# Kernel optimization log

Measured on AMD Instinct MI355X. Metric: run time of the kernel, lower is better.

## Reference

```python
import jax, jax.numpy as jnp
import numpy as np

NEG_SLOPE = 0.01  # torch F.leaky_relu default


def _leaky_relu(v):
    return jnp.where(v >= 0, v, NEG_SLOPE * v)


def _att_layer(t, w1, w2):
    # t: [b, c, n] ; SE-style channel attention with scalar gate
    y = t.mean(axis=-1)                                   # [b, c] (AdaptiveAvgPool1d(1))
    y = jax.nn.sigmoid(jax.nn.relu(y @ w1.T) @ w2.T)       # [b, 1]
    return t * y[:, :, None]


def _avwgcn(x, node_emb, supports, cheb, wpool, bpool, iw, ib, gw, gb,
            a1w1, a1w2, a2w1, a2w2):
    # x: [b, n, c_in]; supports/cheb: [k, n, n]
    b, n, _ = x.shape
    weights = jnp.einsum('nd,dkio->nkio', node_emb, wpool)   # per-node dyn weights
    bias = node_emb @ bpool                                  # [n, o]
    x_g = jnp.einsum('knm,bmc->bnkc', supports, x)           # [b, n, k, c_in]
    x_gconv0 = jnp.einsum('bnki,nkio->bno', x_g, weights) + bias
    x0 = x @ iw.T + ib                                       # init_gconv: [b, n, o]
    x_g1 = jnp.einsum('knm,bmc->bnkc', cheb, x0).reshape(b, n, -1)
    x_gconv1 = x_g1 @ gw.T + gb                              # [b, n, o]
    out = (_att_layer(_leaky_relu(x_gconv0).transpose(0, 2, 1), a1w1, a1w2)
           + _att_layer(_leaky_relu(x_gconv1).transpose(0, 2, 1), a2w1, a2w2))
    return out.transpose(0, 2, 1)                            # [b, n, o]


def _cheb_supports(L, k):
    n = L.shape[0]
    s = [jnp.eye(n, dtype=L.dtype), L]
    for _ in range(2, k):
        s.append(2.0 * L @ s[-1] - s[-2])
    return jnp.stack(s, axis=0)  # [k, n, n]


B, N, DIN, DOUT, K, ED = 64, 1024, 32, 64, 3, 16
CIN = DIN + DOUT  # 96 (gate/update input = cat(x, state))


def setup_inputs() -> dict:
    key = jax.random.key(0)
    ks = jax.random.split(key, 32)
    g = lambda i, shape, s=0.1: jax.random.normal(ks[i], shape, dtype=jnp.float32) * s
    inp = {
        'x': jax.random.normal(ks[0], (B, N, DIN), dtype=jnp.float32),
        'state': jax.random.normal(ks[1], (B, N, DOUT), dtype=jnp.float32),
        'node_embeddings': jax.random.normal(ks[2], (N, ED), dtype=jnp.float32),
        'learned_tilde': jax.random.normal(ks[3], (N, N), dtype=jnp.float32) / np.sqrt(N),
        'cheb_polynomials': jax.random.normal(ks[4], (K, N, N), dtype=jnp.float32) / np.sqrt(N),
        # gate AVWGCN: dim_in=96, dim_out=2*DOUT=128
        'gate_wpool': g(5, (ED, K, CIN, 2 * DOUT)),
        'gate_bpool': g(6, (ED, 2 * DOUT)),
        'gate_iw': g(7, (2 * DOUT, CIN)), 'gate_ib': g(8, (2 * DOUT,)),
        'gate_gw': g(9, (2 * DOUT, 2 * DOUT * K)), 'gate_gb': g(10, (2 * DOUT,)),
        'gate_a1w1': g(11, (2 * DOUT // 16, 2 * DOUT)), 'gate_a1w2': g(12, (1, 2 * DOUT // 16)),
        'gate_a2w1': g(13, (2 * DOUT // 16, 2 * DOUT)), 'gate_a2w2': g(14, (1, 2 * DOUT // 16)),
        # update AVWGCN: dim_in=96, dim_out=DOUT=64
        'upd_wpool': g(15, (ED, K, CIN, DOUT)),
        'upd_bpool': g(16, (ED, DOUT)),
        'upd_iw': g(17, (DOUT, CIN)), 'upd_ib': g(18, (DOUT,)),
        'upd_gw': g(19, (DOUT, DOUT * K)), 'upd_gb': g(20, (DOUT,)),
        'upd_a1w1': g(21, (DOUT // 16, DOUT)), 'upd_a1w2': g(22, (1, DOUT // 16)),
        'upd_a2w1': g(23, (DOUT // 16, DOUT)), 'upd_a2w2': g(24, (1, DOUT // 16)),
    }
    return inp


def reference(x, state, node_embeddings, learned_tilde, cheb_polynomials,
              gate_wpool, gate_bpool, gate_iw, gate_ib, gate_gw, gate_gb,
              gate_a1w1, gate_a1w2, gate_a2w1, gate_a2w2,
              upd_wpool, upd_bpool, upd_iw, upd_ib, upd_gw, upd_gb,
              upd_a1w1, upd_a1w2, upd_a2w1, upd_a2w2):
    supports = _cheb_supports(learned_tilde, K)  # [k, n, n]
    inp_state = jnp.concatenate([x, state], axis=-1)  # [b, n, din+dout]
    z_r = jax.nn.sigmoid(_avwgcn(inp_state, node_embeddings, supports, cheb_polynomials,
                                 gate_wpool, gate_bpool, gate_iw, gate_ib, gate_gw, gate_gb,
                                 gate_a1w1, gate_a1w2, gate_a2w1, gate_a2w2))
    z, r = jnp.split(z_r, 2, axis=-1)
    candidate = jnp.concatenate([x, z * state], axis=-1)
    hc = jnp.tanh(_avwgcn(candidate, node_embeddings, supports, cheb_polynomials,
                          upd_wpool, upd_bpool, upd_iw, upd_ib, upd_gw, upd_gb,
                          upd_a1w1, upd_a1w2, upd_a2w1, upd_a2w2))
    h = r * state + (1.0 - r) * hc
    return h
```

## Files before the change

kernel.cpp:

```cpp
#include <hip/hip_runtime.h>
#include <hip/hip_bf16.h>
#include <math.h>


#define B_  64
#define N_  1024
#define CIN_ 96
#define R_  288

typedef __attribute__((ext_vector_type(8))) short bf16x8;
typedef __attribute__((ext_vector_type(4))) float f32x4;
typedef unsigned short u16;
typedef unsigned int u32;

__device__ __forceinline__ float lrelu(float v) { return v >= 0.f ? v : 0.01f * v; }
__device__ __forceinline__ float sigmoidf_(float u) { return 1.f / (1.f + expf(-u)); }
__device__ __forceinline__ u16 f2b(float f) {
  union { float f; u32 u; } c; c.f = f;
  u32 u = c.u;
  return (u16)((u + 0x7FFFu + ((u >> 16) & 1u)) >> 16);
}
__device__ __forceinline__ float b2f(u16 u) {
  union { u32 x; float f; } c; c.x = ((u32)u) << 16; return c.f;
}
__device__ __forceinline__ void gload_lds16(const u16* gp, u16* lp) {
  __builtin_amdgcn_global_load_lds((const __attribute__((address_space(1))) u32*)gp,
                                   (__attribute__((address_space(3))) u32*)lp, 16, 0, 0);
}

__global__ __launch_bounds__(256) void concat_bf2(const float* __restrict__ x,
                                                  const float* __restrict__ st,
                                                  float* __restrict__ inp,
                                                  u16* __restrict__ inpb) {
  size_t t = (size_t)blockIdx.x * 256 + threadIdx.x;
  if (t >= (size_t)B_ * N_ * CIN_) return;
  int i = (int)(t % CIN_);
  size_t v = t / CIN_;
  size_t b = v & 63, n = v >> 6;
  float f = (i < 32) ? x[(b * N_ + n) * 32 + i] : st[(b * N_ + n) * 64 + (i - 32)];
  inp[t] = f;
  inpb[t] = f2b(f);
}

__global__ __launch_bounds__(256) void conv_f2b(const float* __restrict__ in,
                                                u16* __restrict__ out, int n4) {
  int t = blockIdx.x * 256 + threadIdx.x;
  if (t >= n4) return;
  float4 v = ((const float4*)in)[t];
  ushort4 o;
  o.x = f2b(v.x); o.y = f2b(v.y); o.z = f2b(v.z); o.w = f2b(v.w);
  ((ushort4*)out)[t] = o;
}

__global__ __launch_bounds__(256) void split_hilo(const float* __restrict__ in,
                                                  u16* __restrict__ hi,
                                                  u16* __restrict__ lo, int n4) {
  int t = blockIdx.x * 256 + threadIdx.x;
  if (t >= n4) return;
  float4 v = ((const float4*)in)[t];
  ushort4 h, l;
  h.x = f2b(v.x); l.x = f2b(v.x - b2f(h.x));
  h.y = f2b(v.y); l.y = f2b(v.y - b2f(h.y));
  h.z = f2b(v.z); l.z = f2b(v.z - b2f(h.z));
  h.w = f2b(v.w); l.w = f2b(v.w - b2f(h.w));
  ((ushort4*)hi)[t] = h;
  ((ushort4*)lo)[t] = l;
}

__global__ __launch_bounds__(256) void transpose_split(const float* __restrict__ in,
                                                       u16* __restrict__ hiT,
                                                       u16* __restrict__ loT) {
  __shared__ float t[32][33];
  const int tid = threadIdx.x;
  const int j0 = blockIdx.x * 32, r0 = blockIdx.y * 32;
  const int tc = tid & 31, tr = tid >> 5;
#pragma unroll
  for (int q = 0; q < 4; ++q)
    t[tr + q * 8][tc] = in[(size_t)(r0 + tr + q * 8) * 1024 + j0 + tc];
  __syncthreads();
  const int jj = tid >> 3, rq = (tid & 7) * 4;
  ushort4 h, l;
#pragma unroll
  for (int q = 0; q < 4; ++q) {
    float v = t[rq + q][jj];
    u16 hh = f2b(v);
    ((u16*)&h)[q] = hh;
    ((u16*)&l)[q] = f2b(v - b2f(hh));
  }
  *(ushort4*)(hiT + (size_t)(j0 + jj) * N_ + r0 + rq) = h;
  *(ushort4*)(loT + (size_t)(j0 + jj) * N_ + r0 + rq) = l;
}

__global__ __launch_bounds__(256) void transpose_b2b(const u16* __restrict__ Z, int Zs,
                                                     int Ctot, u16* __restrict__ Zt) {
  __shared__ u16 t[32][36];
  const int tid = threadIdx.x;
  const int c0 = blockIdx.x * 32, n0 = blockIdx.y * 32, b = blockIdx.z;
  {
    const int i = tid >> 3, c4 = (tid & 7) * 4;
    ushort4 v = *(const ushort4*)(Z + ((size_t)(n0 + i) * 64 + b) * Zs + c0 + c4);
    t[i][c4] = v.x; t[i][c4 + 1] = v.y; t[i][c4 + 2] = v.z; t[i][c4 + 3] = v.w;
  }
  __syncthreads();
  {
    const int c = tid >> 3, n4 = (tid & 7) * 4;
    ushort4 o;
    o.x = t[n4][c]; o.y = t[n4 + 1][c]; o.z = t[n4 + 2][c]; o.w = t[n4 + 3][c];
    *(ushort4*)(Zt + (size_t)(b * Ctot + c0 + c) * 1024 + n0 + n4) = o;
  }
}

__global__ __launch_bounds__(256) void wpool_tr(const float* __restrict__ wp,
                                                float* __restrict__ wpT, int OW) {
  __shared__ float t[32][33];
  const int tid = threadIdx.x;
  const int r0 = blockIdx.x * 32, o0 = blockIdx.y * 32, d = blockIdx.z;
  const size_t base = (size_t)d * 288 * OW;
  const int c = tid & 31, q0 = tid >> 5;
#pragma unroll
  for (int q = 0; q < 4; ++q)
    t[q0 + q * 8][c] = wp[base + (size_t)(r0 + q0 + q * 8) * OW + o0 + c];
  __syncthreads();
#pragma unroll
  for (int q = 0; q < 4; ++q)
    wpT[base + (size_t)(o0 + q0 + q * 8) * 288 + r0 + c] = t[c][q0 + q * 8];
}

__global__ __launch_bounds__(256) void mfma_l2p(const u16* __restrict__ Lhi,
                                                const u16* __restrict__ Llo,
                                                const u16* __restrict__ LhiT,
                                                const u16* __restrict__ LloT,
                                                float* __restrict__ P) {
  __shared__ u16 Asl[64 * 64];
  __shared__ u16 Bsl[64 * 64];
  const int tid = threadIdx.x;
  const int w = tid >> 6, lane = tid & 63;
  const int m0 = blockIdx.y * 64, n0 = blockIdx.x * 64;
  const int ph = blockIdx.z;
  const int wr = w >> 1, wc = w & 1;
  const int sr = lane >> 3, so = lane & 7;
  const int cl = lane & 15, q4 = lane >> 4;
  f32x4 acc[2][2] = {};

  const u16* A = (ph == 1) ? Llo : Lhi;
  const u16* B = (ph == 2) ? LloT : LhiT;
  for (int k0 = 0; k0 < 1024; k0 += 64) {
    __syncthreads();
#pragma unroll
    for (int i = 0; i < 2; ++i) {
      const int r = i * 32 + w * 8 + sr;
      const int o = so ^ (r & 7);
      gload_lds16(A + (size_t)(m0 + r) * 1024 + k0 + o * 8, Asl + (i * 32 + w * 8) * 64);
      gload_lds16(B + (size_t)(n0 + r) * 1024 + k0 + o * 8, Bsl + (i * 32 + w * 8) * 64);
    }
    __syncthreads();
#pragma unroll
    for (int kk = 0; kk < 2; ++kk) {
      bf16x8 af[2], bfr[2];
#pragma unroll
      for (int mi = 0; mi < 2; ++mi) {
        const int ra = wr * 32 + mi * 16 + cl;
        af[mi] = *(const bf16x8*)(Asl + ra * 64 + ((kk * 4 + q4) ^ (ra & 7)) * 8);
      }
#pragma unroll
      for (int ni = 0; ni < 2; ++ni) {
        const int rb = wc * 32 + ni * 16 + cl;
        bfr[ni] = *(const bf16x8*)(Bsl + rb * 64 + ((kk * 4 + q4) ^ (rb & 7)) * 8);
      }
#pragma unroll
      for (int mi = 0; mi < 2; ++mi)
#pragma unroll
        for (int ni = 0; ni < 2; ++ni)
          acc[mi][ni] = __builtin_amdgcn_mfma_f32_16x16x32_bf16(af[mi], bfr[ni], acc[mi][ni], 0, 0, 0);
    }
  }
  float* Pz = P + ((size_t)ph << 20);
#pragma unroll
  for (int mi = 0; mi < 2; ++mi)
#pragma unroll
    for (int ni = 0; ni < 2; ++ni) {
      const int j = n0 + wc * 32 + ni * 16 + cl;
#pragma unroll
      for (int r = 0; r < 4; ++r) {
        const int m = m0 + wr * 32 + mi * 16 + q4 * 4 + r;
        Pz[(size_t)m * 1024 + j] = acc[mi][ni][r];
      }
    }
}

__global__ __launch_bounds__(256) void l2_finish(const float* __restrict__ P,
                                                 u16* __restrict__ Y) {
  int t = blockIdx.x * 256 + threadIdx.x;
  float4 a = ((const float4*)P)[t];
  float4 b = ((const float4*)(P + 1048576))[t];
  float4 c = ((const float4*)(P + 2097152))[t];
  int e = t << 2;
  int m = e >> 10, j = e & 1023;
  ushort4 o;
  o.x = f2b(2.f * (a.x + b.x + c.x) - (m == j     ? 1.f : 0.f));
  o.y = f2b(2.f * (a.y + b.y + c.y) - (m == j + 1 ? 1.f : 0.f));
  o.z = f2b(2.f * (a.z + b.z + c.z) - (m == j + 2 ? 1.f : 0.f));
  o.w = f2b(2.f * (a.w + b.w + c.w) - (m == j + 3 ? 1.f : 0.f));
  ((ushort4*)Y)[t] = o;
}

__global__ __launch_bounds__(512) void mfma_stack_w(const u16* __restrict__ A,
                                                    const u16* __restrict__ Bt,
                                                    float* __restrict__ Y, int J) {
  __shared__ u16 Asl[2][128 * 64];
  __shared__ u16 Bsl[2][256 * 64];
  const int tid = threadIdx.x;
  const int w = tid >> 6, lane = tid & 63;
  const int m0 = blockIdx.y * 128, n0 = blockIdx.x * 256;
  const int wr = w >> 2, wc = w & 3;
  const int sr = lane >> 3, so = lane & 7;
  const int cl = lane & 15, q4 = lane >> 4;
  f32x4 acc[4][4] = {};

  auto STAGE = [&](u16* Ad, u16* Bd, int k0) {
#pragma unroll
    for (int i = 0; i < 2; ++i) {
      const int r = i * 64 + w * 8 + sr;
      const int o = so ^ (r & 7);
      gload_lds16(A + (size_t)(m0 + r) * 1024 + k0 + o * 8, Ad + (i * 64 + w * 8) * 64);
    }
#pragma unroll
    for (int i = 0; i < 4; ++i) {
      const int r = i * 64 + w * 8 + sr;
      const int o = so ^ (r & 7);
      gload_lds16(Bt + (size_t)(n0 + r) * 1024 + k0 + o * 8, Bd + (i * 64 + w * 8) * 64);
    }
  };
  auto COMPUTE = [&](const u16* As, const u16* Bs) {
#pragma unroll
    for (int kk = 0; kk < 2; ++kk) {
      bf16x8 af[4], bfr[4];
#pragma unroll
      for (int mi = 0; mi < 4; ++mi) {
        const int ra = wr * 64 + mi * 16 + cl;
        af[mi] = *(const bf16x8*)(As + ra * 64 + ((kk * 4 + q4) ^ (ra & 7)) * 8);
      }
#pragma unroll
      for (int ni = 0; ni < 4; ++ni) {
        const int rb = wc * 64 + ni * 16 + cl;
        bfr[ni] = *(const bf16x8*)(Bs + rb * 64 + ((kk * 4 + q4) ^ (rb & 7)) * 8);
      }
#pragma unroll
      for (int mi = 0; mi < 4; ++mi)
#pragma unroll
        for (int ni = 0; ni < 4; ++ni)
          acc[mi][ni] = __builtin_amdgcn_mfma_f32_16x16x32_bf16(af[mi], bfr[ni], acc[mi][ni], 0, 0, 0);
    }
  };

  STAGE(Asl[0], Bsl[0], 0);
  for (int k0 = 0; k0 < 1024; k0 += 128) {
    STAGE(Asl[1], Bsl[1], k0 + 64);
    asm volatile("s_waitcnt vmcnt(6)" ::: "memory");
    __builtin_amdgcn_s_barrier();
    __builtin_amdgcn_sched_barrier(0);
    COMPUTE(Asl[0], Bsl[0]);
    asm volatile("s_waitcnt lgkmcnt(0)" ::: "memory");
    __builtin_amdgcn_s_barrier();
    __builtin_amdgcn_sched_barrier(0);
    if (k0 + 128 < 1024) {
      STAGE(Asl[0], Bsl[0], k0 + 128);
      asm volatile("s_waitcnt vmcnt(6)" ::: "memory");
    } else {
      asm volatile("s_waitcnt vmcnt(0)" ::: "memory");
    }
    __builtin_amdgcn_s_barrier();
    __builtin_amdgcn_sched_barrier(0);
    COMPUTE(Asl[1], Bsl[1]);
    asm volatile("s_waitcnt lgkmcnt(0)" ::: "memory");
    __builtin_amdgcn_s_barrier();
    __builtin_amdgcn_sched_barrier(0);
  }
#pragma unroll
  for (int mi = 0; mi < 4; ++mi)
#pragma unroll
    for (int ni = 0; ni < 4; ++ni) {
      const int j = n0 + wc * 64 + ni * 16 + cl;
#pragma unroll
      for (int r = 0; r < 4; ++r) {
        const int m = m0 + wr * 64 + mi * 16 + q4 * 4 + r;
        Y[(size_t)m * J + j] = acc[mi][ni][r];
      }
    }
}

template <int O, int OSH>
__global__ __launch_bounds__(128) void vgen2(const float* __restrict__ gw,
                                             const float* __restrict__ iw,
                                             const float* __restrict__ ib,
                                             int Ctot,
                                             u16* __restrict__ Vb,
                                             float* __restrict__ ball) {
  const int c = blockIdx.x;
  const int col = threadIdx.x;
  if (c >= Ctot) {
    if (col < 96) Vb[(size_t)c * 96 + col] = 0;
    else if (col == 96) ball[c] = 0.f;
    return;
  }
  __shared__ float sg[O];
  const int o = c & (O - 1), k = c >> OSH;
  const float* g = gw + (size_t)o * (3 * O) + (size_t)k * O;
  for (int e = col; e < O; e += 128) sg[e] = g[e];
  __syncthreads();
  if (col < 96) {
    float s = 0.f;
#pragma unroll
    for (int j = 0; j < O; ++j) s += sg[j] * iw[j * 96 + col];
    Vb[(size_t)c * 96 + col] = f2b(s);
  } else if (col == 96) {
    float s = 0.f;
#pragma unroll
    for (int j = 0; j < O; ++j) s += sg[j] * ib[j];
    ball[c] = s;
  }
}

__global__ __launch_bounds__(256) void zgemm(const u16* __restrict__ A,
                                             const u16* __restrict__ Bt,
                                             const float* __restrict__ ball,
                                             u16* __restrict__ Z, int Zs) {
  __shared__ u16 Asl[128 * 32];
  __shared__ u16 Bsl[128 * 32];
  const int tid = threadIdx.x;
  const int w = tid >> 6, lane = tid & 63;
  const int m0 = blockIdx.y * 128, n0 = blockIdx.x * 128;
  const int wr = w >> 1, wc = w & 1;
  const int sr = lane >> 2, so = lane & 3;
  const int cl = lane & 15, q4 = lane >> 4;
  f32x4 acc[4][4] = {};
  for (int k0 = 0; k0 < 96; k0 += 32) {
    __syncthreads();
#pragma unroll
    for (int i = 0; i < 2; ++i) {
      const int r = i * 64 + w * 16 + sr;
      const int o = so ^ (r & 3);
      gload_lds16(A + (size_t)(m0 + r) * 96 + k0 + o * 8, Asl + (i * 64 + w * 16) * 32);
      gload_lds16(Bt + (size_t)(n0 + r) * 96 + k0 + o * 8, Bsl + (i * 64 + w * 16) * 32);
    }
    __syncthreads();
    bf16x8 af[4], bfr[4];
#pragma unroll
    for (int mi = 0; mi < 4; ++mi) {
      const int ra = wr * 64 + mi * 16 + cl;
      af[mi] = *(const bf16x8*)(Asl + ra * 32 + (q4 ^ (ra & 3)) * 8);
    }
#pragma unroll
    for (int ni = 0; ni < 4; ++ni) {
      const int rb = wc * 64 + ni * 16 + cl;
      bfr[ni] = *(const bf16x8*)(Bsl + rb * 32 + (q4 ^ (rb & 3)) * 8);
    }
#pragma unroll
    for (int mi = 0; mi < 4; ++mi)
#pragma unroll
      for (int ni = 0; ni < 4; ++ni)
        acc[mi][ni] = __builtin_amdgcn_mfma_f32_16x16x32_bf16(af[mi], bfr[ni], acc[mi][ni], 0, 0, 0);
  }
#pragma unroll
  for (int mi = 0; mi < 4; ++mi)
#pragma unroll
    for (int ni = 0; ni < 4; ++ni) {
      const int c = n0 + wc * 64 + ni * 16 + cl;
      const float bb = ball[c];
#pragma unroll
      for (int r = 0; r < 4; ++r) {
        const int m = m0 + wr * 64 + mi * 16 + q4 * 4 + r;
        Z[(size_t)m * Zs + c] = f2b(acc[mi][ni][r] + bb);
      }
    }
}

__global__ __launch_bounds__(512) void mfma_k3(const u16* __restrict__ A3,
                                               const u16* __restrict__ Zt,
                                               const float* __restrict__ gb,
                                               float* __restrict__ Y,
                                               int J, int obits) {
  __shared__ u16 Asl[2][128 * 64];
  __shared__ u16 Bsl[2][128 * 64];
  const int tid = threadIdx.x;
  const int w = tid >> 6, lane = tid & 63;
  const int m0 = blockIdx.y * 128, n0 = blockIdx.x * 128;
  const int wr = w >> 2, wc = w & 3;
  const int sr = lane >> 3, so = lane & 7;
  const int cl = lane & 15, q4 = lane >> 4;
  const int omask = (1 << obits) - 1;
  f32x4 acc[4][2] = {};

  auto STAGE = [&](u16* Ad, u16* Bd, int k0) {
    const int kb = k0 >> 10, ko = k0 & 1023;
#pragma unroll
    for (int i = 0; i < 2; ++i) {
      const int r = i * 64 + w * 8 + sr;
      const int o = so ^ (r & 7);
      gload_lds16(A3 + (size_t)kb * 1048576 + (size_t)(m0 + r) * 1024 + ko + o * 8,
                  Ad + (i * 64 + w * 8) * 64);
      const int jp = n0 + r;
      const int brow = (((jp >> obits) * 3 + kb) << obits) | (jp & omask);
      gload_lds16(Zt + (size_t)brow * 1024 + ko + o * 8, Bd + (i * 64 + w * 8) * 64);
    }
  };
  auto COMPUTE = [&](const u16* As, const u16* Bs) {
#pragma unroll
    for (int kk = 0; kk < 2; ++kk) {
      bf16x8 af[4], bfr[2];
#pragma unroll
      for (int mi = 0; mi < 4; ++mi) {
        const int ra = wr * 64 + mi * 16 + cl;
        af[mi] = *(const bf16x8*)(As + ra * 64 + ((kk * 4 + q4) ^ (ra & 7)) * 8);
      }
#pragma unroll
      for (int ni = 0; ni < 2; ++ni) {
        const int rb = wc * 32 + ni * 16 + cl;
        bfr[ni] = *(const bf16x8*)(Bs + rb * 64 + ((kk * 4 + q4) ^ (rb & 7)) * 8);
      }
#pragma unroll
      for (int mi = 0; mi < 4; ++mi)
#pragma unroll
        for (int ni = 0; ni < 2; ++ni)
          acc[mi][ni] = __builtin_amdgcn_mfma_f32_16x16x32_bf16(af[mi], bfr[ni], acc[mi][ni], 0, 0, 0);
    }
  };

  STAGE(Asl[0], Bsl[0], 0);
  for (int k0 = 0; k0 < 3072; k0 += 128) {
    STAGE(Asl[1], Bsl[1], k0 + 64);
    asm volatile("s_waitcnt vmcnt(4)" ::: "memory");
    __builtin_amdgcn_s_barrier();
    __builtin_amdgcn_sched_barrier(0);
    COMPUTE(Asl[0], Bsl[0]);
    asm volatile("s_waitcnt lgkmcnt(0)" ::: "memory");
    __builtin_amdgcn_s_barrier();
    __builtin_amdgcn_sched_barrier(0);
    if (k0 + 128 < 3072) {
      STAGE(Asl[0], Bsl[0], k0 + 128);
      asm volatile("s_waitcnt vmcnt(4)" ::: "memory");
    } else {
      asm volatile("s_waitcnt vmcnt(0)" ::: "memory");
    }
    __builtin_amdgcn_s_barrier();
    __builtin_amdgcn_sched_barrier(0);
    COMPUTE(Asl[1], Bsl[1]);
    asm volatile("s_waitcnt lgkmcnt(0)" ::: "memory");
    __builtin_amdgcn_s_barrier();
    __builtin_amdgcn_sched_barrier(0);
  }
#pragma unroll
  for (int mi = 0; mi < 4; ++mi)
#pragma unroll
    for (int ni = 0; ni < 2; ++ni) {
      const int j = n0 + wc * 32 + ni * 16 + cl;
      const float bb = gb[j & omask];
#pragma unroll
      for (int r = 0; r < 4; ++r) {
        const int m = m0 + wr * 64 + mi * 16 + q4 * 4 + r;
        Y[(size_t)m * J + j] = acc[mi][ni][r] + bb;
      }
    }
}

__global__ __launch_bounds__(512) void mfma_k3w(const u16* __restrict__ A3,
                                                const u16* __restrict__ Zt,
                                                const float* __restrict__ gb,
                                                float* __restrict__ Y,
                                                int J, int obits) {
  __shared__ u16 Asl[2][128 * 64];
  __shared__ u16 Bsl[2][256 * 64];
  const int tid = threadIdx.x;
  const int w = tid >> 6, lane = tid & 63;
  const int m0 = blockIdx.y * 128, n0 = blockIdx.x * 256;
  const int wr = w >> 2, wc = w & 3;
  const int sr = lane >> 3, so = lane & 7;
  const int cl = lane & 15, q4 = lane >> 4;
  const int omask = (1 << obits) - 1;
  f32x4 acc[4][4] = {};

  auto STAGE = [&](u16* Ad, u16* Bd, int k0) {
    const int kb = k0 >> 10, ko = k0 & 1023;
#pragma unroll
    for (int i = 0; i < 2; ++i) {
      const int r = i * 64 + w * 8 + sr;
      const int o = so ^ (r & 7);
      gload_lds16(A3 + (size_t)kb * 1048576 + (size_t)(m0 + r) * 1024 + ko + o * 8,
                  Ad + (i * 64 + w * 8) * 64);
    }
#pragma unroll
    for (int i = 0; i < 4; ++i) {
      const int r = i * 64 + w * 8 + sr;
      const int o = so ^ (r & 7);
      const int jp = n0 + r;
      const int brow = (((jp >> obits) * 3 + kb) << obits) | (jp & omask);
      gload_lds16(Zt + (size_t)brow * 1024 + ko + o * 8, Bd + (i * 64 + w * 8) * 64);
    }
  };
  auto COMPUTE = [&](const u16* As, const u16* Bs) {
#pragma unroll
    for (int kk = 0; kk < 2; ++kk) {
      bf16x8 af[4], bfr[4];
#pragma unroll
      for (int mi = 0; mi < 4; ++mi) {
        const int ra = wr * 64 + mi * 16 + cl;
        af[mi] = *(const bf16x8*)(As + ra * 64 + ((kk * 4 + q4) ^ (ra & 7)) * 8);
      }
#pragma unroll
      for (int ni = 0; ni < 4; ++ni) {
        const int rb = wc * 64 + ni * 16 + cl;
        bfr[ni] = *(const bf16x8*)(Bs + rb * 64 + ((kk * 4 + q4) ^ (rb & 7)) * 8);
      }
#pragma unroll
      for (int mi = 0; mi < 4; ++mi)
#pragma unroll
        for (int ni = 0; ni < 4; ++ni)
          acc[mi][ni] = __builtin_amdgcn_mfma_f32_16x16x32_bf16(af[mi], bfr[ni], acc[mi][ni], 0, 0, 0);
    }
  };

  STAGE(Asl[0], Bsl[0], 0);
  for (int k0 = 0; k0 < 3072; k0 += 128) {
    STAGE(Asl[1], Bsl[1], k0 + 64);
    asm volatile("s_waitcnt vmcnt(6)" ::: "memory");
    __builtin_amdgcn_s_barrier();
    __builtin_amdgcn_sched_barrier(0);
    COMPUTE(Asl[0], Bsl[0]);
    asm volatile("s_waitcnt lgkmcnt(0)" ::: "memory");
    __builtin_amdgcn_s_barrier();
    __builtin_amdgcn_sched_barrier(0);
    if (k0 + 128 < 3072) {
      STAGE(Asl[0], Bsl[0], k0 + 128);
      asm volatile("s_waitcnt vmcnt(6)" ::: "memory");
    } else {
      asm volatile("s_waitcnt vmcnt(0)" ::: "memory");
    }
    __builtin_amdgcn_s_barrier();
    __builtin_amdgcn_sched_barrier(0);
    COMPUTE(Asl[1], Bsl[1]);
    asm volatile("s_waitcnt lgkmcnt(0)" ::: "memory");
    __builtin_amdgcn_s_barrier();
    __builtin_amdgcn_sched_barrier(0);
  }
#pragma unroll
  for (int mi = 0; mi < 4; ++mi)
#pragma unroll
    for (int ni = 0; ni < 4; ++ni) {
      const int j = n0 + wc * 64 + ni * 16 + cl;
      const float bb = gb[j & omask];
#pragma unroll
      for (int r = 0; r < 4; ++r) {
        const int m = m0 + wr * 64 + mi * 16 + q4 * 4 + r;
        Y[(size_t)m * J + j] = acc[mi][ni][r] + bb;
      }
    }
}

template <int SZ>
__global__ __launch_bounds__(256) void weightgen5(const float* __restrict__ emb,
                                                  const float* __restrict__ wpT,
                                                  u16* __restrict__ W) {
  const int tid = threadIdx.x;
  const int ro = blockIdx.x * 256 + tid;
  const int n0 = blockIdx.y * 64;
  __shared__ float semb[64][17];
  for (int e = tid; e < 1024; e += 256) semb[e >> 4][e & 15] = emb[(n0 + (e >> 4)) * 16 + (e & 15)];
  __syncthreads();
  float wv[16];
#pragma unroll
  for (int d = 0; d < 16; ++d) wv[d] = wpT[(size_t)d * SZ + ro];
#pragma unroll 4
  for (int n = 0; n < 64; ++n) {
    float s = 0.f;
#pragma unroll
    for (int d = 0; d < 16; ++d) s += semb[n][d] * wv[d];
    W[(size_t)(n0 + n) * SZ + ro] = f2b(s);
  }
}

template <int OW>
__global__ __launch_bounds__(256) void pernode10(const float* __restrict__ xa,
                                                 const float* __restrict__ xbc,
                                                 const u16* __restrict__ Wt,
                                                 const float* __restrict__ emb,
                                                 const float* __restrict__ bpool,
                                                 float* __restrict__ outp) {
  constexpr int MT = OW / 64;
  const int n = blockIdx.x;
  const int tid = threadIdx.x;
  const int w = tid >> 6, lane = tid & 63;
  const int cl = lane & 15, q4 = lane >> 4;
  __shared__ u16 sWt[OW * 32];
  __shared__ u16 sXh[64 * 32];
  __shared__ u16 sXl[64 * 32];
  __shared__ float semb[16];
  if (tid < 16) semb[tid] = emb[n * 16 + tid];
  f32x4 acc[MT][4] = {};
  const u16* Wn = Wt + (size_t)n * (OW * 288);
  const int xb = tid >> 2, rg = tid & 3;

  for (int c = 0; c < 9; ++c) {
    const int k = c / 3, i0 = (c % 3) * 32;
    const float* xk = (k == 0) ? (xa + (size_t)n * 6144)
                               : (xbc + ((size_t)(k - 1) * 1024 + n) * 6144);
    __syncthreads();
#pragma unroll
    for (int i = 0; i < MT; ++i) {
      const int g = w * MT + i;
      const int o = g * 16 + (lane >> 2);
      const int seg = (lane & 3) ^ (o & 3);
      gload_lds16(Wn + (size_t)o * 288 + c * 32 + seg * 8, sWt + g * 512);
    }
    {
      const float* p = xk + (size_t)xb * 96 + i0 + rg * 8;
      float4 v0 = *(const float4*)p;
      float4 v1 = *(const float4*)(p + 4);
      float xv[8] = {v0.x, v0.y, v0.z, v0.w, v1.x, v1.y, v1.z, v1.w};
      bf16x8 h, l;
#pragma unroll
      for (int j = 0; j < 8; ++j) {
        u16 hh = f2b(xv[j]);
        ((u16*)&h)[j] = hh;
        ((u16*)&l)[j] = f2b(xv[j] - b2f(hh));
      }
      const int col = (rg ^ (xb & 3)) * 8;
      *(bf16x8*)(sXh + xb * 32 + col) = h;
      *(bf16x8*)(sXl + xb * 32 + col) = l;
    }
    __syncthreads();
    bf16x8 aw[MT], bh[4], bl[4];
#pragma unroll
    for (int mi = 0; mi < MT; ++mi) {
      const int o = (w * MT + mi) * 16 + cl;
      aw[mi] = *(const bf16x8*)(sWt + o * 32 + ((q4 ^ (o & 3)) * 8));
    }
#pragma unroll
    for (int ni = 0; ni < 4; ++ni) {
      const int b = ni * 16 + cl;
      const int col = (q4 ^ (b & 3)) * 8;
      bh[ni] = *(const bf16x8*)(sXh + b * 32 + col);
      bl[ni] = *(const bf16x8*)(sXl + b * 32 + col);
    }
#pragma unroll
    for (int mi = 0; mi < MT; ++mi)
#pragma unroll
      for (int ni = 0; ni < 4; ++ni)
        acc[mi][ni] = __builtin_amdgcn_mfma_f32_16x16x32_bf16(aw[mi], bh[ni], acc[mi][ni], 0, 0, 0);
#pragma unroll
    for (int mi = 0; mi < MT; ++mi)
#pragma unroll
      for (int ni = 0; ni < 4; ++ni)
        acc[mi][ni] = __builtin_amdgcn_mfma_f32_16x16x32_bf16(aw[mi], bl[ni], acc[mi][ni], 0, 0, 0);
  }
  float4 biasv[MT];
#pragma unroll
  for (int mi = 0; mi < MT; ++mi)
#pragma unroll
    for (int r = 0; r < 4; ++r) {
      const int o = (w * MT + mi) * 16 + q4 * 4 + r;
      float s = 0.f;
#pragma unroll
      for (int d = 0; d < 16; ++d) s += semb[d] * bpool[d * OW + o];
      ((float*)&biasv[mi])[r] = s;
    }
#pragma unroll
  for (int mi = 0; mi < MT; ++mi)
#pragma unroll
    for (int ni = 0; ni < 4; ++ni) {
      const int b = ni * 16 + cl;
      float4 v;
      v.x = acc[mi][ni][0] + biasv[mi].x;
      v.y = acc[mi][ni][1] + biasv[mi].y;
      v.z = acc[mi][ni][2] + biasv[mi].z;
      v.w = acc[mi][ni][3] + biasv[mi].w;
      *(float4*)(outp + ((size_t)n * 64 + b) * OW + (w * MT + mi) * 16 + q4 * 4) = v;
    }
}

template <int C>
__global__ __launch_bounds__(256) void att_reduce(const float* __restrict__ A0,
                                                  const float* __restrict__ A1,
                                                  float* __restrict__ part0,
                                                  float* __restrict__ part1) {
  constexpr int C4 = C / 4;
  constexpr int H = 256 / C4;
  const int chunk = blockIdx.x;
  const int b = blockIdx.y;
  const int tid = threadIdx.x;
  const int c4 = tid % C4, h = tid / C4;
  __shared__ float4 r0[256], r1[256];
  float4 s0 = {0.f, 0.f, 0.f, 0.f}, s1 = {0.f, 0.f, 0.f, 0.f};
  const float4* p0 = (const float4*)(A0 + (size_t)b * C) + c4;
  const float4* p1 = (const float4*)(A1 + (size_t)b * C) + c4;
  const size_t stride = (size_t)B_ * C4;
  for (int n = chunk * 64 + h; n < chunk * 64 + 64; n += H) {
    float4 v0 = p0[(size_t)n * stride];
    float4 v1 = p1[(size_t)n * stride];
    s0.x += lrelu(v0.x); s0.y += lrelu(v0.y); s0.z += lrelu(v0.z); s0.w += lrelu(v0.w);
    s1.x += lrelu(v1.x); s1.y += lrelu(v1.y); s1.z += lrelu(v1.z); s1.w += lrelu(v1.w);
  }
  r0[tid] = s0; r1[tid] = s1;
  __syncthreads();
  if (h == 0) {
    for (int hh = 1; hh < H; ++hh) {
      float4 a = r0[c4 + hh * C4], bb = r1[c4 + hh * C4];
      s0.x += a.x; s0.y += a.y; s0.z += a.z; s0.w += a.w;
      s1.x += bb.x; s1.y += bb.y; s1.z += bb.z; s1.w += bb.w;
    }
    ((float4*)(part0 + ((size_t)b * 16 + chunk) * C))[c4] = s0;
    ((float4*)(part1 + ((size_t)b * 16 + chunk) * C))[c4] = s1;
  }
}

template <int C, int HID>
__global__ __launch_bounds__(256) void att_finish(const float* __restrict__ part0,
                                                  const float* __restrict__ part1,
                                                  const float* __restrict__ w11,
                                                  const float* __restrict__ w12,
                                                  const float* __restrict__ w21,
                                                  const float* __restrict__ w22,
                                                  float* __restrict__ sout) {
  const int b = blockIdx.x;
  const int tid = threadIdx.x;
  __shared__ float sm0[C], sm1[C];
  __shared__ float h0[HID], h1[HID];
  if (tid < C) {
    float s0 = 0.f, s1 = 0.f;
    for (int ch = 0; ch < 16; ++ch) {
      s0 += part0[((size_t)b * 16 + ch) * C + tid];
      s1 += part1[((size_t)b * 16 + ch) * C + tid];
    }
    sm0[tid] = s0 * (1.f / N_); sm1[tid] = s1 * (1.f / N_);
  }
  __syncthreads();
  if (tid < HID) {
    float a = 0.f;
    for (int cc = 0; cc < C; ++cc) a += sm0[cc] * w11[tid * C + cc];
    h0[tid] = fmaxf(a, 0.f);
  } else if (tid >= 32 && tid < 32 + HID) {
    int j = tid - 32;
    float a = 0.f;
    for (int cc = 0; cc < C; ++cc) a += sm1[cc] * w21[j * C + cc];
    h1[j] = fmaxf(a, 0.f);
  }
  __syncthreads();
  if (tid == 0) {
    float a = 0.f;
    for (int j = 0; j < HID; ++j) a += h0[j] * w12[j];
    sout[b] = sigmoidf_(a);
  } else if (tid == 32) {
    float a = 0.f;
    for (int j = 0; j < HID; ++j) a += h1[j] * w22[j];
    sout[B_ + b] = sigmoidf_(a);
  }
}

__global__ __launch_bounds__(256) void gate_combine_b2(const float* __restrict__ a0,
                                                       const float* __restrict__ a1,
                                                       const float* __restrict__ s12,
                                                       const float* __restrict__ x,
                                                       const float* __restrict__ st,
                                                       float* __restrict__ cand,
                                                       u16* __restrict__ candb,
                                                       float* __restrict__ rbuf) {
  size_t t = (size_t)blockIdx.x * 256 + threadIdx.x;
  if (t >= (size_t)B_ * N_ * 64) return;
  int c = (int)(t & 63);
  int b = (int)((t >> 6) & 63);
  int n = (int)(t >> 12);
  float s1 = s12[b], s2 = s12[B_ + b];
  size_t nb = (size_t)n * B_ + b;
  size_t i128 = nb * 128;
  float uz = s1 * lrelu(a0[i128 + c]) + s2 * lrelu(a1[i128 + c]);
  float ur = s1 * lrelu(a0[i128 + 64 + c]) + s2 * lrelu(a1[i128 + 64 + c]);
  float z = sigmoidf_(uz);
  float r = sigmoidf_(ur);
  float stv = st[((size_t)b * N_ + n) * 64 + c];
  float zs = z * stv;
  cand[nb * CIN_ + 32 + c] = zs;
  candb[nb * CIN_ + 32 + c] = f2b(zs);
  rbuf[nb * 64 + c] = r;
  if (c < 32) {
    float xv = x[((size_t)b * N_ + n) * 32 + c];
    cand[nb * CIN_ + c] = xv;
    candb[nb * CIN_ + c] = f2b(xv);
  }
}

__global__ __launch_bounds__(256) void final_h(const float* __restrict__ a0,
                                               const float* __restrict__ a1,
                                               const float* __restrict__ s12,
                                               const float* __restrict__ rbuf,
                                               const float* __restrict__ st,
                                               float* __restrict__ out) {
  size_t t = (size_t)blockIdx.x * 256 + threadIdx.x;
  if (t >= (size_t)B_ * N_ * 64) return;
  int o = (int)(t & 63);
  int n = (int)((t >> 6) & 1023);
  int b = (int)(t >> 16);
  float s1 = s12[b], s2 = s12[B_ + b];
  size_t nb = ((size_t)n * B_ + b) * 64 + o;
  float u = s1 * lrelu(a0[nb]) + s2 * lrelu(a1[nb]);
  float hc = tanhf(u);
  float r = rbuf[nb];
  out[t] = r * st[t] + (1.f - r) * hc;
}

extern "C" void kernel_launch(void* const* d_in, const int* in_sizes, int n_in,
                              void* d_out, int out_size, void* d_ws, size_t ws_size,
                              hipStream_t stream) {
  const float* x       = (const float*)d_in[0];
  const float* state   = (const float*)d_in[1];
  const float* emb     = (const float*)d_in[2];
  const float* Ltil    = (const float*)d_in[3];
  const float* cheb    = (const float*)d_in[4];
  const float* g_wpool = (const float*)d_in[5];
  const float* g_bpool = (const float*)d_in[6];
  const float* g_iw    = (const float*)d_in[7];
  const float* g_ib    = (const float*)d_in[8];
  const float* g_gw    = (const float*)d_in[9];
  const float* g_gb    = (const float*)d_in[10];
  const float* g_a1w1  = (const float*)d_in[11];
  const float* g_a1w2  = (const float*)d_in[12];
  const float* g_a2w1  = (const float*)d_in[13];
  const float* g_a2w2  = (const float*)d_in[14];
  const float* u_wpool = (const float*)d_in[15];
  const float* u_bpool = (const float*)d_in[16];
  const float* u_iw    = (const float*)d_in[17];
  const float* u_ib    = (const float*)d_in[18];
  const float* u_gw    = (const float*)d_in[19];
  const float* u_gb    = (const float*)d_in[20];
  const float* u_a1w1  = (const float*)d_in[21];
  const float* u_a1w2  = (const float*)d_in[22];
  const float* u_a2w1  = (const float*)d_in[23];
  const float* u_a2w2  = (const float*)d_in[24];
  float* out = (float*)d_out;

  float* ws    = (float*)d_ws;
  float* inp   = ws;
  u16*   inpb  = (u16*)(ws + 6291456);
  float* t12   = ws + 9437184;
  u16*   Zbuf  = (u16*)t12;
  u16*   Wbuf  = (u16*)(ws + 22020096);
  u16*   Wbuf128 = Wbuf;
  u16*   Btp   = (u16*)(ws + 31457280);
  u16*   Zt    = Wbuf;
  float* acc1  = ws + 34603008;
  float* acc0  = ws + 42991616;
  u16*   LbStk = (u16*)(ws + 51380224);
  u16*   chebb = (u16*)(ws + 52428800);
  float* s12   = ws + 54001664;
  float* s12u  = ws + 54001792;
  float* part0 = ws + 54001920;
  float* part1 = ws + 54132992;
  float* rbuf  = ws + 54264064;
  u16*   Vbg   = (u16*)(ws + 58458368);
  float* bag   = ws + 58476800;
  u16*   Vbu   = (u16*)(ws + 58477184);
  float* bau   = ws + 58489472;
  u16*   LhiT  = (u16*)(ws + 58489728);
  u16*   LloT  = (u16*)(ws + 59014016);
  u16*   Llo   = (u16*)(ws + 59538304);
  float* wpTg  = ws + 58489728;
  float* wpTu  = ws + 59079552;

  dim3 blk(256);
  dim3 blk512(512);

  split_hilo<<<1024, blk, 0, stream>>>(Ltil, LbStk, Llo, 262144);
  transpose_split<<<dim3(32, 32), blk, 0, stream>>>(Ltil, LhiT, LloT);
  mfma_l2p<<<dim3(16, 16, 3), blk, 0, stream>>>(LbStk, Llo, LhiT, LloT, t12);
  wpool_tr<<<dim3(9, 4, 16), blk, 0, stream>>>(g_wpool, wpTg, 128);
  wpool_tr<<<dim3(9, 2, 16), blk, 0, stream>>>(u_wpool, wpTu, 64);
  l2_finish<<<1024, blk, 0, stream>>>(t12, LbStk + 1048576);
  conv_f2b<<<3072, blk, 0, stream>>>(cheb, chebb, 786432);

  concat_bf2<<<24576, blk, 0, stream>>>(x, state, inp, inpb);
  transpose_b2b<<<dim3(3, 32, 64), blk, 0, stream>>>(inpb, 96, 96, Btp);
  mfma_stack_w<<<dim3(24, 16), blk512, 0, stream>>>(LbStk, Btp, t12, 6144);
  vgen2<128, 7><<<384, dim3(128), 0, stream>>>(g_gw, g_iw, g_ib, 384, Vbg, bag);
  weightgen5<36864><<<dim3(144, 16), blk, 0, stream>>>(emb, wpTg, Wbuf128);
  pernode10<128><<<1024, blk, 0, stream>>>(inp, t12, Wbuf128, emb, g_bpool, acc0);
  zgemm<<<dim3(3, 512), blk, 0, stream>>>(inpb, Vbg, bag, Zbuf, 384);
  transpose_b2b<<<dim3(12, 32, 64), blk, 0, stream>>>(Zbuf, 384, 384, Zt);
  mfma_k3w<<<dim3(32, 8), blk512, 0, stream>>>(chebb, Zt, g_gb, acc1, 8192, 7);
  att_reduce<128><<<dim3(16, 64), blk, 0, stream>>>(acc0, acc1, part0, part1);
  att_finish<128, 8><<<64, blk, 0, stream>>>(part0, part1, g_a1w1, g_a1w2, g_a2w1, g_a2w2, s12);
  gate_combine_b2<<<16384, blk, 0, stream>>>(acc0, acc1, s12, x, state, inp, inpb, rbuf);

  transpose_b2b<<<dim3(3, 32, 64), blk, 0, stream>>>(inpb, 96, 96, Btp);
  mfma_stack_w<<<dim3(24, 16), blk512, 0, stream>>>(LbStk, Btp, t12, 6144);
  vgen2<64, 6><<<256, dim3(128), 0, stream>>>(u_gw, u_iw, u_ib, 192, Vbu, bau);
  weightgen5<18432><<<dim3(72, 16), blk, 0, stream>>>(emb, wpTu, Wbuf);
  pernode10<64><<<1024, blk, 0, stream>>>(inp, t12, Wbuf, emb, u_bpool, acc0);
  zgemm<<<dim3(2, 512), blk, 0, stream>>>(inpb, Vbu, bau, Zbuf, 256);
  transpose_b2b<<<dim3(6, 32, 64), blk, 0, stream>>>(Zbuf, 256, 192, Zt);
  mfma_k3<<<dim3(32, 8), blk512, 0, stream>>>(chebb, Zt, u_gb, acc1, 4096, 6);
  att_reduce<64><<<dim3(16, 64), blk, 0, stream>>>(acc0, acc1, part0, part1);
  att_finish<64, 4><<<64, blk, 0, stream>>>(part0, part1, u_a1w1, u_a1w2, u_a2w1, u_a2w2, s12u);
  final_h<<<16384, blk, 0, stream>>>(acc0, acc1, s12u, rbuf, state, out);
}
```

Measured before the change: 631.2 us.

## Split-K the Chebyshev MFMA GEMMs into two halves and fold partials downstream

Both Chebyshev-graph GEMM kernels now run with a grid z-dimension of two, each half covering half of the 3072-long K range. The second half writes an fp32 partial buffer that the attention reduce, gate-combine and final kernels add in. The goal is to double the number of workgroups (the original grids had only 256) to better fill the GPU. The wide variant also halves its K tile to 32, which cuts LDS use per block. The cost is writing and re-reading an extra fp32 partial tensor, and Pk aliases t12/Zbuf, so buffer lifetimes must not overlap.

```diff
diff --git a/kernel.cpp b/kernel.cpp
--- a/kernel.cpp
+++ b/kernel.cpp
@@ -375,24 +375,26 @@
     }
 }
 
-__global__ __launch_bounds__(512) void mfma_k3(const u16* __restrict__ A3,
-                                               const u16* __restrict__ Zt,
-                                               const float* __restrict__ gb,
-                                               float* __restrict__ Y,
-                                               int J, int obits) {
+__global__ __launch_bounds__(512) void mfma_k3s(const u16* __restrict__ A3,
+                                                const u16* __restrict__ Zt,
+                                                const float* __restrict__ gb,
+                                                float* __restrict__ Y,
+                                                float* __restrict__ P1,
+                                                int J, int obits) {
   __shared__ u16 Asl[2][128 * 64];
   __shared__ u16 Bsl[2][128 * 64];
   const int tid = threadIdx.x;
   const int w = tid >> 6, lane = tid & 63;
   const int m0 = blockIdx.y * 128, n0 = blockIdx.x * 128;
+  const int kh = blockIdx.z;
   const int wr = w >> 2, wc = w & 3;
   const int sr = lane >> 3, so = lane & 7;
   const int cl = lane & 15, q4 = lane >> 4;
   const int omask = (1 << obits) - 1;
   f32x4 acc[4][2] = {};
 
-  auto STAGE = [&](u16* Ad, u16* Bd, int k0) {
-    const int kb = k0 >> 10, ko = k0 & 1023;
+  auto STAGE = [&](u16* Ad, u16* Bd, int kg) {
+    const int kb = kg >> 10, ko = kg & 1023;
 #pragma unroll
     for (int i = 0; i < 2; ++i) {
       const int r = i * 64 + w * 8 + sr;
@@ -426,9 +428,10 @@
     }
   };
 
-  STAGE(Asl[0], Bsl[0], 0);
-  for (int k0 = 0; k0 < 3072; k0 += 128) {
-    STAGE(Asl[1], Bsl[1], k0 + 64);
+  const int kbase = kh * 1536;
+  STAGE(Asl[0], Bsl[0], kbase);
+  for (int k0 = 0; k0 < 1536; k0 += 128) {
+    STAGE(Asl[1], Bsl[1], kbase + k0 + 64);
     asm volatile("s_waitcnt vmcnt(4)" ::: "memory");
     __builtin_amdgcn_s_barrier();
     __builtin_amdgcn_sched_barrier(0);
@@ -436,8 +439,8 @@
     asm volatile("s_waitcnt lgkmcnt(0)" ::: "memory");
     __builtin_amdgcn_s_barrier();
     __builtin_amdgcn_sched_barrier(0);
-    if (k0 + 128 < 3072) {
-      STAGE(Asl[0], Bsl[0], k0 + 128);
+    if (k0 + 128 < 1536) {
+      STAGE(Asl[0], Bsl[0], kbase + k0 + 128);
       asm volatile("s_waitcnt vmcnt(4)" ::: "memory");
     } else {
       asm volatile("s_waitcnt vmcnt(0)" ::: "memory");
@@ -454,84 +457,84 @@
 #pragma unroll
     for (int ni = 0; ni < 2; ++ni) {
       const int j = n0 + wc * 32 + ni * 16 + cl;
-      const float bb = gb[j & omask];
+      const float bb = (kh == 0) ? gb[j & omask] : 0.f;
+      float* dst = (kh == 0) ? Y : P1;
 #pragma unroll
       for (int r = 0; r < 4; ++r) {
         const int m = m0 + wr * 64 + mi * 16 + q4 * 4 + r;
-        Y[(size_t)m * J + j] = acc[mi][ni][r] + bb;
-      }
-    }
-}
-
-__global__ __launch_bounds__(512) void mfma_k3w(const u16* __restrict__ A3,
-                                                const u16* __restrict__ Zt,
-                                                const float* __restrict__ gb,
-                                                float* __restrict__ Y,
-                                                int J, int obits) {
-  __shared__ u16 Asl[2][128 * 64];
-  __shared__ u16 Bsl[2][256 * 64];
+        dst[(size_t)m * J + j] = acc[mi][ni][r] + bb;
+      }
+    }
+}
+
+__global__ __launch_bounds__(512) void mfma_k3ws(const u16* __restrict__ A3,
+                                                 const u16* __restrict__ Zt,
+                                                 const float* __restrict__ gb,
+                                                 float* __restrict__ Y,
+                                                 float* __restrict__ P1,
+                                                 int J, int obits) {
+  __shared__ u16 Asl[2][128 * 32];
+  __shared__ u16 Bsl[2][256 * 32];
   const int tid = threadIdx.x;
   const int w = tid >> 6, lane = tid & 63;
   const int m0 = blockIdx.y * 128, n0 = blockIdx.x * 256;
+  const int kh = blockIdx.z;
   const int wr = w >> 2, wc = w & 3;
-  const int sr = lane >> 3, so = lane & 7;
+  const int rr = lane >> 2, seg = lane & 3;
   const int cl = lane & 15, q4 = lane >> 4;
   const int omask = (1 << obits) - 1;
   f32x4 acc[4][4] = {};
 
-  auto STAGE = [&](u16* Ad, u16* Bd, int k0) {
-    const int kb = k0 >> 10, ko = k0 & 1023;
+  auto STAGE = [&](u16* Ad, u16* Bd, int kg) {
+    const int kb = kg >> 10, ko = kg & 1023;
+    {
+      const int r = w * 16 + rr;
+      const int o = seg ^ (r & 3);
+      gload_lds16(A3 + (size_t)kb * 1048576 + (size_t)(m0 + r) * 1024 + ko + o * 8,
+                  Ad + w * 512);
+    }
 #pragma unroll
     for (int i = 0; i < 2; ++i) {
-      const int r = i * 64 + w * 8 + sr;
-      const int o = so ^ (r & 7);
-      gload_lds16(A3 + (size_t)kb * 1048576 + (size_t)(m0 + r) * 1024 + ko + o * 8,
-                  Ad + (i * 64 + w * 8) * 64);
-    }
-#pragma unroll
-    for (int i = 0; i < 4; ++i) {
-      const int r = i * 64 + w * 8 + sr;
-      const int o = so ^ (r & 7);
+      const int r = i * 128 + w * 16 + rr;
+      const int o = seg ^ (r & 3);
       const int jp = n0 + r;
       const int brow = (((jp >> obits) * 3 + kb) << obits) | (jp & omask);
-      gload_lds16(Zt + (size_t)brow * 1024 + ko + o * 8, Bd + (i * 64 + w * 8) * 64);
+      gload_lds16(Zt + (size_t)brow * 1024 + ko + o * 8, Bd + i * 4096 + w * 512);
     }
   };
   auto COMPUTE = [&](const u16* As, const u16* Bs) {
-#pragma unroll
-    for (int kk = 0; kk < 2; ++kk) {
-      bf16x8 af[4], bfr[4];
-#pragma unroll
-      for (int mi = 0; mi < 4; ++mi) {
-        const int ra = wr * 64 + mi * 16 + cl;
-        af[mi] = *(const bf16x8*)(As + ra * 64 + ((kk * 4 + q4) ^ (ra & 7)) * 8);
-      }
-#pragma unroll
-      for (int ni = 0; ni < 4; ++ni) {
-        const int rb = wc * 64 + ni * 16 + cl;
-        bfr[ni] = *(const bf16x8*)(Bs + rb * 64 + ((kk * 4 + q4) ^ (rb & 7)) * 8);
-      }
-#pragma unroll
-      for (int mi = 0; mi < 4; ++mi)
-#pragma unroll
-        for (int ni = 0; ni < 4; ++ni)
-          acc[mi][ni] = __builtin_amdgcn_mfma_f32_16x16x32_bf16(af[mi], bfr[ni], acc[mi][ni], 0, 0, 0);
-    }
+    bf16x8 af[4], bfr[4];
+#pragma unroll
+    for (int mi = 0; mi < 4; ++mi) {
+      const int ra = wr * 64 + mi * 16 + cl;
+      af[mi] = *(const bf16x8*)(As + ra * 32 + ((q4 ^ (ra & 3)) * 8));
+    }
+#pragma unroll
+    for (int ni = 0; ni < 4; ++ni) {
+      const int rb = wc * 64 + ni * 16 + cl;
+      bfr[ni] = *(const bf16x8*)(Bs + rb * 32 + ((q4 ^ (rb & 3)) * 8));
+    }
+#pragma unroll
+    for (int mi = 0; mi < 4; ++mi)
+#pragma unroll
+      for (int ni = 0; ni < 4; ++ni)
+        acc[mi][ni] = __builtin_amdgcn_mfma_f32_16x16x32_bf16(af[mi], bfr[ni], acc[mi][ni], 0, 0, 0);
   };
 
-  STAGE(Asl[0], Bsl[0], 0);
-  for (int k0 = 0; k0 < 3072; k0 += 128) {
-    STAGE(Asl[1], Bsl[1], k0 + 64);
-    asm volatile("s_waitcnt vmcnt(6)" ::: "memory");
+  const int kbase = kh * 1536;
+  STAGE(Asl[0], Bsl[0], kbase);
+  for (int k0 = 0; k0 < 1536; k0 += 64) {
+    STAGE(Asl[1], Bsl[1], kbase + k0 + 32);
+    asm volatile("s_waitcnt vmcnt(3)" ::: "memory");
     __builtin_amdgcn_s_barrier();
     __builtin_amdgcn_sched_barrier(0);
     COMPUTE(Asl[0], Bsl[0]);
     asm volatile("s_waitcnt lgkmcnt(0)" ::: "memory");
     __builtin_amdgcn_s_barrier();
     __builtin_amdgcn_sched_barrier(0);
-    if (k0 + 128 < 3072) {
-      STAGE(Asl[0], Bsl[0], k0 + 128);
-      asm volatile("s_waitcnt vmcnt(6)" ::: "memory");
+    if (k0 + 64 < 1536) {
+      STAGE(Asl[0], Bsl[0], kbase + k0 + 64);
+      asm volatile("s_waitcnt vmcnt(3)" ::: "memory");
     } else {
       asm volatile("s_waitcnt vmcnt(0)" ::: "memory");
     }
@@ -547,11 +550,12 @@
 #pragma unroll
     for (int ni = 0; ni < 4; ++ni) {
       const int j = n0 + wc * 64 + ni * 16 + cl;
-      const float bb = gb[j & omask];
+      const float bb = (kh == 0) ? gb[j & omask] : 0.f;
+      float* dst = (kh == 0) ? Y : P1;
 #pragma unroll
       for (int r = 0; r < 4; ++r) {
         const int m = m0 + wr * 64 + mi * 16 + q4 * 4 + r;
-        Y[(size_t)m * J + j] = acc[mi][ni][r] + bb;
+        dst[(size_t)m * J + j] = acc[mi][ni][r] + bb;
       }
     }
 }
@@ -680,6 +684,7 @@
 template <int C>
 __global__ __launch_bounds__(256) void att_reduce(const float* __restrict__ A0,
                                                   const float* __restrict__ A1,
+                                                  const float* __restrict__ PZ,
                                                   float* __restrict__ part0,
                                                   float* __restrict__ part1) {
   constexpr int C4 = C / 4;
@@ -692,12 +697,15 @@
   float4 s0 = {0.f, 0.f, 0.f, 0.f}, s1 = {0.f, 0.f, 0.f, 0.f};
   const float4* p0 = (const float4*)(A0 + (size_t)b * C) + c4;
   const float4* p1 = (const float4*)(A1 + (size_t)b * C) + c4;
+  const float4* pz = (const float4*)(PZ + (size_t)b * C) + c4;
   const size_t stride = (size_t)B_ * C4;
   for (int n = chunk * 64 + h; n < chunk * 64 + 64; n += H) {
     float4 v0 = p0[(size_t)n * stride];
     float4 v1 = p1[(size_t)n * stride];
+    float4 u1 = pz[(size_t)n * stride];
     s0.x += lrelu(v0.x); s0.y += lrelu(v0.y); s0.z += lrelu(v0.z); s0.w += lrelu(v0.w);
-    s1.x += lrelu(v1.x); s1.y += lrelu(v1.y); s1.z += lrelu(v1.z); s1.w += lrelu(v1.w);
+    s1.x += lrelu(v1.x + u1.x); s1.y += lrelu(v1.y + u1.y);
+    s1.z += lrelu(v1.z + u1.z); s1.w += lrelu(v1.w + u1.w);
   }
   r0[tid] = s0; r1[tid] = s1;
   __syncthreads();
@@ -757,6 +765,7 @@
 
 __global__ __launch_bounds__(256) void gate_combine_b2(const float* __restrict__ a0,
                                                        const float* __restrict__ a1,
+                                                       const float* __restrict__ pz,
                                                        const float* __restrict__ s12,
                                                        const float* __restrict__ x,
                                                        const float* __restrict__ st,
@@ -771,8 +780,8 @@
   float s1 = s12[b], s2 = s12[B_ + b];
   size_t nb = (size_t)n * B_ + b;
   size_t i128 = nb * 128;
-  float uz = s1 * lrelu(a0[i128 + c]) + s2 * lrelu(a1[i128 + c]);
-  float ur = s1 * lrelu(a0[i128 + 64 + c]) + s2 * lrelu(a1[i128 + 64 + c]);
+  float uz = s1 * lrelu(a0[i128 + c]) + s2 * lrelu(a1[i128 + c] + pz[i128 + c]);
+  float ur = s1 * lrelu(a0[i128 + 64 + c]) + s2 * lrelu(a1[i128 + 64 + c] + pz[i128 + 64 + c]);
   float z = sigmoidf_(uz);
   float r = sigmoidf_(ur);
   float stv = st[((size_t)b * N_ + n) * 64 + c];
@@ -789,6 +798,7 @@
 
 __global__ __launch_bounds__(256) void final_h(const float* __restrict__ a0,
                                                const float* __restrict__ a1,
+                                               const float* __restrict__ pz,
                                                const float* __restrict__ s12,
                                                const float* __restrict__ rbuf,
                                                const float* __restrict__ st,
@@ -800,7 +810,7 @@
   int b = (int)(t >> 16);
   float s1 = s12[b], s2 = s12[B_ + b];
   size_t nb = ((size_t)n * B_ + b) * 64 + o;
-  float u = s1 * lrelu(a0[nb]) + s2 * lrelu(a1[nb]);
+  float u = s1 * lrelu(a0[nb]) + s2 * lrelu(a1[nb] + pz[nb]);
   float hc = tanhf(u);
   float r = rbuf[nb];
   out[t] = r * st[t] + (1.f - r) * hc;
@@ -841,6 +851,7 @@
   u16*   inpb  = (u16*)(ws + 6291456);
   float* t12   = ws + 9437184;
   u16*   Zbuf  = (u16*)t12;
+  float* Pk    = t12;
   u16*   Wbuf  = (u16*)(ws + 22020096);
   u16*   Wbuf128 = Wbuf;
   u16*   Btp   = (u16*)(ws + 31457280);
@@ -883,10 +894,10 @@
   pernode10<128><<<1024, blk, 0, stream>>>(inp, t12, Wbuf128, emb, g_bpool, acc0);
   zgemm<<<dim3(3, 512), blk, 0, stream>>>(inpb, Vbg, bag, Zbuf, 384);
   transpose_b2b<<<dim3(12, 32, 64), blk, 0, stream>>>(Zbuf, 384, 384, Zt);
-  mfma_k3w<<<dim3(32, 8), blk512, 0, stream>>>(chebb, Zt, g_gb, acc1, 8192, 7);
-  att_reduce<128><<<dim3(16, 64), blk, 0, stream>>>(acc0, acc1, part0, part1);
+  mfma_k3ws<<<dim3(32, 8, 2), blk512, 0, stream>>>(chebb, Zt, g_gb, acc1, Pk, 8192, 7);
+  att_reduce<128><<<dim3(16, 64), blk, 0, stream>>>(acc0, acc1, Pk, part0, part1);
   att_finish<128, 8><<<64, blk, 0, stream>>>(part0, part1, g_a1w1, g_a1w2, g_a2w1, g_a2w2, s12);
-  gate_combine_b2<<<16384, blk, 0, stream>>>(acc0, acc1, s12, x, state, inp, inpb, rbuf);
+  gate_combine_b2<<<16384, blk, 0, stream>>>(acc0, acc1, Pk, s12, x, state, inp, inpb, rbuf);
 
   transpose_b2b<<<dim3(3, 32, 64), blk, 0, stream>>>(inpb, 96, 96, Btp);
   mfma_stack_w<<<dim3(24, 16), blk512, 0, stream>>>(LbStk, Btp, t12, 6144);
@@ -895,8 +906,8 @@
   pernode10<64><<<1024, blk, 0, stream>>>(inp, t12, Wbuf, emb, u_bpool, acc0);
   zgemm<<<dim3(2, 512), blk, 0, stream>>>(inpb, Vbu, bau, Zbuf, 256);
   transpose_b2b<<<dim3(6, 32, 64), blk, 0, stream>>>(Zbuf, 256, 192, Zt);
-  mfma_k3<<<dim3(32, 8), blk512, 0, stream>>>(chebb, Zt, u_gb, acc1, 4096, 6);
-  att_reduce<64><<<dim3(16, 64), blk, 0, stream>>>(acc0, acc1, part0, part1);
+  mfma_k3s<<<dim3(32, 8, 2), blk512, 0, stream>>>(chebb, Zt, u_gb, acc1, Pk, 4096, 6);
+  att_reduce<64><<<dim3(16, 64), blk, 0, stream>>>(acc0, acc1, Pk, part0, part1);
   att_finish<64, 4><<<64, blk, 0, stream>>>(part0, part1, u_a1w1, u_a1w2, u_a2w1, u_a2w2, s12u);
-  final_h<<<16384, blk, 0, stream>>>(acc0, acc1, s12u, rbuf, state, out);
-}
+  final_h<<<16384, blk, 0, stream>>>(acc0, acc1, Pk, s12u, rbuf, state, out);
+}
```

Result: no change. 640.8 us (+1.5%).
